# Performance work log

Hardware: AMD Instinct MI355X
Metric: run time of the kernel (lower is better)

## Reference

```python
import jax, jax.numpy as jnp
import numpy as np

N_NODES = 2000
N_EDGES = 32000
B, T = 16, 20
OUT = 8      # GAT out_feats (num_heads=1)
HID = 24     # LSTM hidden
FC_OUT = 160  # num_airports * prediction_horizon = 20*8
FCC_OUT = 20
NEG_SLOPE = 0.2


def setup_inputs() -> dict:
    key = jax.random.key(0)
    ks = jax.random.split(key, 20)
    s = 0.1
    return {
        "x": jax.random.normal(ks[0], (B, T, N_NODES, 1), jnp.float32),
        "edge_w": jax.random.uniform(ks[1], (B, T, N_EDGES, 1), jnp.float32),
        "src": jax.random.randint(ks[2], (N_EDGES,), 0, N_NODES, dtype=jnp.int32),
        "dst": jax.random.randint(ks[3], (N_EDGES,), 0, N_NODES, dtype=jnp.int32),
        # EdgeGATConv params
        "W_node": jax.random.normal(ks[4], (1, OUT), jnp.float32) * s,
        "W_edge": jax.random.normal(ks[5], (1, OUT), jnp.float32) * s,
        "attn_l": jax.random.normal(ks[6], (OUT,), jnp.float32) * s,
        "attn_e": jax.random.normal(ks[7], (OUT,), jnp.float32) * s,
        "attn_r": jax.random.normal(ks[8], (OUT,), jnp.float32) * s,
        "gat_b": jnp.zeros((OUT,), jnp.float32),
        # LSTM params (PyTorch gate order i,f,g,o)
        "w_ih": jax.random.normal(ks[9], (4 * HID, OUT), jnp.float32) * s,
        "w_hh": jax.random.normal(ks[10], (4 * HID, HID), jnp.float32) * s,
        "b_ih": jnp.zeros((4 * HID,), jnp.float32),
        "b_hh": jnp.zeros((4 * HID,), jnp.float32),
        # fc / fcc
        "fc_w": jax.random.normal(ks[11], (FC_OUT, HID), jnp.float32) * s,
        "fc_b": jnp.zeros((FC_OUT,), jnp.float32),
        "fcc_w": jax.random.normal(ks[12], (FCC_OUT, 8 * 20), jnp.float32) * s,
        "fcc_b": jnp.zeros((FCC_OUT,), jnp.float32),
    }


def _gat_graph(xg, wg, src, dst, W_node, W_edge, attn_l, attn_e, attn_r, gat_b):
    # xg: [N,1], wg: [E,1] -> pooled graph feature [OUT]
    fs = xg @ W_node                      # [N,OUT] projected node feats
    fe = wg @ W_edge                      # [E,OUT] projected edge feats
    el = fs @ attn_l                      # [N]
    er = fs @ attn_r                      # [N]  (dst == src features, homogeneous graph)
    ee = fe @ attn_e                      # [E]
    e = jax.nn.leaky_relu(el[src] + ee + er[dst], NEG_SLOPE)  # [E]
    # edge_softmax over incoming edges of each dst node
    emax = jax.ops.segment_max(e, dst, num_segments=N_NODES)  # [N]
    num = jnp.exp(e - emax[dst])
    den = jax.ops.segment_sum(num, dst, num_segments=N_NODES)
    a = num / den[dst]                    # [E]
    msg = a[:, None] * (fs[src] + fe)     # [E,OUT]
    rst = jax.ops.segment_sum(msg, dst, num_segments=N_NODES) + gat_b  # [N,OUT]
    return rst.mean(axis=0)               # graph mean-pool -> [OUT]


def reference(x, edge_w, src, dst, W_node, W_edge, attn_l, attn_e, attn_r, gat_b,
              w_ih, w_hh, b_ih, b_hh, fc_w, fc_b, fcc_w, fcc_b):
    # GAT per (series, time) graph, vmapped over flattened B*T axis
    xf = x.reshape(B * T, N_NODES, 1)
    wf = edge_w.reshape(B * T, N_EDGES, 1)
    gat = jax.vmap(lambda xg, wg: _gat_graph(xg, wg, src, dst, W_node, W_edge,
                                             attn_l, attn_e, attn_r, gat_b))
    feats = gat(xf, wf).reshape(B, T, OUT)  # [B,T,8]
    # Dropout(0.1) -> identity in eval mode

    # LSTM (batch_first), zero initial state
    def step(carry, xt):
        h, c = carry
        g = xt @ w_ih.T + h @ w_hh.T + b_ih + b_hh  # [B,4H]
        i, f, gg, o = jnp.split(g, 4, axis=-1)
        c = jax.nn.sigmoid(f) * c + jax.nn.sigmoid(i) * jnp.tanh(gg)
        h = jax.nn.sigmoid(o) * jnp.tanh(c)
        return (h, c), h

    h0 = jnp.zeros((B, HID), feats.dtype)
    (_, _), hs = jax.lax.scan(step, (h0, h0), jnp.swapaxes(feats, 0, 1))
    outputs = jnp.swapaxes(hs, 0, 1)      # [B,T,24]; squeeze(0) is a no-op for B>1

    out = outputs @ fc_w.T + fc_b         # [B,T,160]
    out = out.reshape(-1, 8 * 20) @ fcc_w.T + fcc_b  # [B*T,20]
    return out
```

## Files before the change

kernel.cpp:

```cpp
#include <hip/hip_runtime.h>
#include <math.h>

#define N_NODES 2000
#define N_EDGES 32000
#define BB 16
#define TT 20
#define NG (BB*TT)
#define OUTF 8
#define HID 24
#define FC_OUTD 160
#define FCC_OUTD 20

#define SC_DEN 4194304.0f
#define SC_T1  1048576.0f
#define SC_T2  4194304.0f



__global__ __launch_bounds__(1024) void gat_fused(
    const float* __restrict__ x, const float* __restrict__ edge_w,
    const int* __restrict__ src, const int* __restrict__ dst,
    const float* __restrict__ W_node, const float* __restrict__ W_edge,
    const float* __restrict__ attn_l, const float* __restrict__ attn_e,
    const float* __restrict__ attn_r, const float* __restrict__ gat_b,
    const float* __restrict__ fc_w, const float* __restrict__ fc_b,
    const float* __restrict__ fcc_w, const float* __restrict__ fcc_b,
    float* __restrict__ ws)
{
    __shared__ float xs[N_NODES];
    __shared__ int   aden[N_NODES];
    __shared__ int   at1[N_NODES];
    __shared__ int   at2[N_NODES];
    __shared__ double wr1[16], wr2[16];

    const int tid = threadIdx.x;

    if (blockIdx.x == NG) {
        if (tid < FCC_OUTD * HID) {
            int j = tid / HID, h = tid % HID;
            float acc = 0.f;
#pragma unroll 4
            for (int m = 0; m < FC_OUTD; ++m)
                acc += fcc_w[j * FC_OUTD + m] * fc_w[m * HID + h];
            ws[NG * OUTF + tid] = acc;
        } else if (tid < FCC_OUTD * HID + FCC_OUTD) {
            int j = tid - FCC_OUTD * HID;
            float acc = fcc_b[j];
#pragma unroll 4
            for (int m = 0; m < FC_OUTD; ++m)
                acc += fcc_w[j * FC_OUTD + m] * fc_b[m];
            ws[NG * OUTF + FCC_OUTD * HID + j] = acc;
        }
        return;
    }

    const int g = blockIdx.x;

    float cl = 0.f, ce = 0.f, cr = 0.f;
#pragma unroll
    for (int k = 0; k < OUTF; ++k) {
        cl += W_node[k] * attn_l[k];
        cr += W_node[k] * attn_r[k];
        ce += W_edge[k] * attn_e[k];
    }

    const float* xg = x + (size_t)g * N_NODES;
    const float* wg = edge_w + (size_t)g * N_EDGES;

    {
        const float4* xg4 = (const float4*)xg;
        for (int i = tid; i < N_NODES/4; i += 1024)
            ((float4*)xs)[i] = xg4[i];
        for (int i = tid; i < N_NODES; i += 1024) {
            aden[i] = 0; at1[i] = 0; at2[i] = 0;
        }
    }
    __syncthreads();

    const int4*   src4 = (const int4*)src;
    const int4*   dst4 = (const int4*)dst;
    const float4* wg4  = (const float4*)wg;
#pragma unroll
    for (int k = 0; k < (N_EDGES/4 + 1023) / 1024; ++k) {
        int c = tid + k * 1024;
        if (c < N_EDGES/4) {
            int4   sv = src4[c];
            int4   dv = dst4[c];
            float4 wv = wg4[c];
#pragma unroll
            for (int j = 0; j < 4; ++j) {
                int   s = (&sv.x)[j];
                int   d = (&dv.x)[j];
                float w = (&wv.x)[j];
                float xsv = xs[s];
                float ev  = cl * xsv + ce * w + cr * xs[d];
                ev = fmaxf(ev, 0.2f * ev);
                float num = __expf(ev);
                atomicAdd(&aden[d], __float2int_rn(num * SC_DEN));
                atomicAdd(&at1[d],  __float2int_rn(num * xsv * SC_T1));
                atomicAdd(&at2[d],  __float2int_rn(num * w * SC_T2));
            }
        }
    }
    __syncthreads();

    double s1 = 0.0, s2 = 0.0;
    for (int n = tid; n < N_NODES; n += 1024) {
        int deni = aden[n];
        if (deni > 0) {
            double inv = 1.0 / (double)deni;
            s1 += (double)at1[n] * 4.0 * inv;
            s2 += (double)at2[n] * inv;
        }
    }
#pragma unroll
    for (int off = 32; off > 0; off >>= 1) {
        s1 += __shfl_down(s1, off, 64);
        s2 += __shfl_down(s2, off, 64);
    }
    int wave = tid >> 6, lane = tid & 63;
    if (lane == 0) { wr1[wave] = s1; wr2[wave] = s2; }
    __syncthreads();
    if (tid == 0) {
        double a = 0.0, c = 0.0;
#pragma unroll
        for (int w = 0; w < 16; ++w) { a += wr1[w]; c += wr2[w]; }
#pragma unroll
        for (int k = 0; k < OUTF; ++k)
            ws[g * OUTF + k] = gat_b[k] +
                (float)((a * (double)W_node[k] + c * (double)W_edge[k]) / (double)N_NODES);
    }
}


__device__ __forceinline__ float fast_sigmoid(float v) {
    return 1.f / (1.f + __expf(-v));
}
__device__ __forceinline__ float fast_tanh(float v) {
    float t = __expf(2.f * v);
    return (t - 1.f) / (t + 1.f);
}

__global__ __launch_bounds__(128) void lstm_head(
    const float* __restrict__ ws,
    const float* __restrict__ w_ih, const float* __restrict__ w_hh,
    const float* __restrict__ b_ih, const float* __restrict__ b_hh,
    float* __restrict__ out)
{
    __shared__ float s_M[FCC_OUTD * HID];
    __shared__ float s_b2[FCC_OUTD];
    __shared__ float s_xt[TT * OUTF];
    __shared__ float s_bias[96];
    __shared__ float s_xg[TT * 96];
    __shared__ float s_g[96];
    __shared__ float s_h[HID], s_c[HID];
    __shared__ float s_hs[TT * HID];

    const int b   = blockIdx.x;
    const int tid = threadIdx.x;

    for (int i = tid; i < FCC_OUTD * HID; i += 128) s_M[i]  = ws[NG * OUTF + i];
    if (tid < FCC_OUTD) s_b2[tid] = ws[NG * OUTF + FCC_OUTD * HID + tid];
    for (int i = tid; i < TT * OUTF; i += 128) s_xt[i] = ws[b * TT * OUTF + i];
    if (tid < 96) s_bias[tid] = b_ih[tid] + b_hh[tid];
    if (tid < HID) { s_h[tid] = 0.f; s_c[tid] = 0.f; }

    float rw_hh[HID];
    if (tid < 96) {
#pragma unroll
        for (int k = 0; k < HID; ++k) rw_hh[k] = w_hh[tid * HID + k];
    }
    __syncthreads();

    for (int u = tid; u < TT * 96; u += 128) {
        int t = u / 96, j = u % 96;
        float acc = s_bias[j];
        const float* xt = &s_xt[t * OUTF];
#pragma unroll
        for (int k = 0; k < OUTF; ++k) acc += xt[k] * w_ih[j * OUTF + k];
        s_xg[u] = acc;
    }
    __syncthreads();

    for (int t = 0; t < TT; ++t) {
        if (tid < 96) {
            float acc = s_xg[t * 96 + tid];
#pragma unroll
            for (int k = 0; k < HID; ++k) acc += s_h[k] * rw_hh[k];
            s_g[tid] = acc;
        }
        __syncthreads();
        if (tid < HID) {
            float i_ = fast_sigmoid(s_g[tid]);
            float f_ = fast_sigmoid(s_g[24 + tid]);
            float g_ = fast_tanh(s_g[48 + tid]);
            float o_ = fast_sigmoid(s_g[72 + tid]);
            float c = f_ * s_c[tid] + i_ * g_;
            s_c[tid] = c;
            float h = o_ * fast_tanh(c);
            s_h[tid] = h;
            s_hs[t * HID + tid] = h;
        }
        __syncthreads();
    }

    for (int u = tid; u < TT * FCC_OUTD; u += 128) {
        int t = u / FCC_OUTD, j = u % FCC_OUTD;
        float acc = s_b2[j];
        const float* hr = &s_hs[t * HID];
#pragma unroll
        for (int h = 0; h < HID; ++h) acc += hr[h] * s_M[j * HID + h];
        out[(b * TT + t) * FCC_OUTD + j] = acc;
    }
}

extern "C" void kernel_launch(void* const* d_in, const int* in_sizes, int n_in,
                              void* d_out, int out_size, void* d_ws, size_t ws_size,
                              hipStream_t stream) {
    const float* x      = (const float*)d_in[0];
    const float* edge_w = (const float*)d_in[1];
    const int*   src    = (const int*)d_in[2];
    const int*   dst    = (const int*)d_in[3];
    const float* W_node = (const float*)d_in[4];
    const float* W_edge = (const float*)d_in[5];
    const float* attn_l = (const float*)d_in[6];
    const float* attn_e = (const float*)d_in[7];
    const float* attn_r = (const float*)d_in[8];
    const float* gat_b  = (const float*)d_in[9];
    const float* w_ih   = (const float*)d_in[10];
    const float* w_hh   = (const float*)d_in[11];
    const float* b_ih   = (const float*)d_in[12];
    const float* b_hh   = (const float*)d_in[13];
    const float* fc_w   = (const float*)d_in[14];
    const float* fc_b   = (const float*)d_in[15];
    const float* fcc_w  = (const float*)d_in[16];
    const float* fcc_b  = (const float*)d_in[17];

    float* ws  = (float*)d_ws;
    float* out = (float*)d_out;

    gat_fused<<<NG + 1, 1024, 0, stream>>>(x, edge_w, src, dst, W_node, W_edge,
                                           attn_l, attn_e, attn_r, gat_b,
                                           fc_w, fc_b, fcc_w, fcc_b, ws);
    lstm_head<<<BB, 128, 0, stream>>>(ws, w_ih, w_hh, b_ih, b_hh, out);
}
```

Baseline: 45.82 us.

## Replace LDS atomic scatter with per-call CSR build and segmented reduction

Adds two small kernels that build a dst-sorted CSR layout each call: a histogram plus prefix scan, then a scatter that records each edge's sorted position and packed src/dst/head-flag metadata. The GAT kernel scatters edge weights into LDS in sorted order and has 1000 threads each reduce 32 consecutive edges with float accumulators. Partial segments that cross thread boundaries are stitched afterwards, replacing the three fixed-point LDS atomics per edge. This trades atomic contention for two extra launches, a 128KB LDS buffer per block that limits occupancy, and only 1000 of 1024 threads active in the main loop.

```diff
diff --git a/kernel.cpp b/kernel.cpp
--- a/kernel.cpp
+++ b/kernel.cpp
@@ -10,51 +10,99 @@
 #define HID 24
 #define FC_OUTD 160
 #define FCC_OUTD 20
-
-#define SC_DEN 4194304.0f
-#define SC_T1  1048576.0f
-#define SC_T2  4194304.0f
-
-
-
-__global__ __launch_bounds__(1024) void gat_fused(
-    const float* __restrict__ x, const float* __restrict__ edge_w,
+#define EPT 32
+#define NTE (N_EDGES/EPT)
+
+#define WS_CSRPOS   0
+#define WS_META     131072
+#define WS_ROWPTR   262144
+#define WS_CURSOR   270336
+#define WS_FEATS    278528
+#define WS_M        290816
+#define WS_B2       292864
+
+
+__global__ __launch_bounds__(1024) void build_hist_scan(
+    const int* __restrict__ dst, int* __restrict__ row_ptr, int* __restrict__ cursor)
+{
+    __shared__ int a[2048], b[2048];
+    const int tid = threadIdx.x;
+    a[tid] = 0; a[tid + 1024] = 0;
+    __syncthreads();
+    for (int e = tid; e < N_EDGES; e += 1024) atomicAdd(&a[dst[e]], 1);
+    __syncthreads();
+    int *s = a, *d = b;
+    for (int off = 1; off < 2048; off <<= 1) {
+        d[tid] = s[tid] + (tid >= off ? s[tid - off] : 0);
+        const int j = tid + 1024;
+        d[j] = s[j] + (j >= off ? s[j - off] : 0);
+        __syncthreads();
+        int* t = s; s = d; d = t;
+    }
+    if (tid == 0) row_ptr[0] = 0;
+    for (int i = tid; i < N_NODES; i += 1024) {
+        row_ptr[i + 1] = s[i];
+        cursor[i] = 0;
+    }
+}
+
+
+__global__ __launch_bounds__(1024) void build_scatter(
     const int* __restrict__ src, const int* __restrict__ dst,
-    const float* __restrict__ W_node, const float* __restrict__ W_edge,
-    const float* __restrict__ attn_l, const float* __restrict__ attn_e,
-    const float* __restrict__ attn_r, const float* __restrict__ gat_b,
+    const int* __restrict__ row_ptr, int* __restrict__ cursor,
+    unsigned* __restrict__ meta, unsigned* __restrict__ csr_pos,
     const float* __restrict__ fc_w, const float* __restrict__ fc_b,
     const float* __restrict__ fcc_w, const float* __restrict__ fcc_b,
-    float* __restrict__ ws)
+    float* __restrict__ Mout, float* __restrict__ b2out)
 {
-    __shared__ float xs[N_NODES];
-    __shared__ int   aden[N_NODES];
-    __shared__ int   at1[N_NODES];
-    __shared__ int   at2[N_NODES];
-    __shared__ double wr1[16], wr2[16];
-
     const int tid = threadIdx.x;
-
-    if (blockIdx.x == NG) {
+    if (blockIdx.x == 32) {
         if (tid < FCC_OUTD * HID) {
-            int j = tid / HID, h = tid % HID;
+            const int j = tid / HID, h = tid % HID;
             float acc = 0.f;
 #pragma unroll 4
             for (int m = 0; m < FC_OUTD; ++m)
                 acc += fcc_w[j * FC_OUTD + m] * fc_w[m * HID + h];
-            ws[NG * OUTF + tid] = acc;
+            Mout[tid] = acc;
         } else if (tid < FCC_OUTD * HID + FCC_OUTD) {
-            int j = tid - FCC_OUTD * HID;
+            const int j = tid - FCC_OUTD * HID;
             float acc = fcc_b[j];
 #pragma unroll 4
             for (int m = 0; m < FC_OUTD; ++m)
                 acc += fcc_w[j * FC_OUTD + m] * fc_b[m];
-            ws[NG * OUTF + FCC_OUTD * HID + j] = acc;
+            b2out[j] = acc;
         }
         return;
     }
-
-    const int g = blockIdx.x;
+    const int e = blockIdx.x * 1024 + tid;
+    if (e >= N_EDGES) return;
+    const int s = src[e], d = dst[e];
+    const int rp  = row_ptr[d];
+    const int pos = rp + atomicAdd(&cursor[d], 1);
+    const unsigned fl = (pos == rp) ? 1u : 0u;
+    const unsigned m  = (unsigned)s | ((unsigned)d << 11) | (fl << 22);
+    const int t = pos >> 5, i = pos & 31;
+    meta[(((i >> 2) * NTE) + t) * 4 + (i & 3)] = m;
+    csr_pos[e] = (unsigned)pos;
+}
+
+
+__global__ __launch_bounds__(1024) void gat_csr(
+    const float* __restrict__ x, const float* __restrict__ edge_w,
+    const unsigned* __restrict__ csr_pos, const int4* __restrict__ meta4,
+    const float* __restrict__ W_node, const float* __restrict__ W_edge,
+    const float* __restrict__ attn_l, const float* __restrict__ attn_e,
+    const float* __restrict__ attn_r, const float* __restrict__ gat_b,
+    float* __restrict__ feats)
+{
+    __shared__ float wsp[N_EDGES];
+    __shared__ float xs[N_NODES];
+    __shared__ int   hn[NTE];
+    __shared__ float hp0[NTE], hp1[NTE], hp2[NTE];
+    __shared__ double wr1[16], wr2[16];
+
+    const int g   = blockIdx.x;
+    const int tid = threadIdx.x;
 
     float cl = 0.f, ce = 0.f, cr = 0.f;
 #pragma unroll
@@ -64,61 +112,83 @@
         ce += W_edge[k] * attn_e[k];
     }
 
-    const float* xg = x + (size_t)g * N_NODES;
-    const float* wg = edge_w + (size_t)g * N_EDGES;
-
     {
-        const float4* xg4 = (const float4*)xg;
-        for (int i = tid; i < N_NODES/4; i += 1024)
-            ((float4*)xs)[i] = xg4[i];
-        for (int i = tid; i < N_NODES; i += 1024) {
-            aden[i] = 0; at1[i] = 0; at2[i] = 0;
-        }
-    }
-    __syncthreads();
-
-    const int4*   src4 = (const int4*)src;
-    const int4*   dst4 = (const int4*)dst;
-    const float4* wg4  = (const float4*)wg;
-#pragma unroll
-    for (int k = 0; k < (N_EDGES/4 + 1023) / 1024; ++k) {
-        int c = tid + k * 1024;
-        if (c < N_EDGES/4) {
-            int4   sv = src4[c];
-            int4   dv = dst4[c];
-            float4 wv = wg4[c];
-#pragma unroll
-            for (int j = 0; j < 4; ++j) {
-                int   s = (&sv.x)[j];
-                int   d = (&dv.x)[j];
-                float w = (&wv.x)[j];
-                float xsv = xs[s];
-                float ev  = cl * xsv + ce * w + cr * xs[d];
-                ev = fmaxf(ev, 0.2f * ev);
-                float num = __expf(ev);
-                atomicAdd(&aden[d], __float2int_rn(num * SC_DEN));
-                atomicAdd(&at1[d],  __float2int_rn(num * xsv * SC_T1));
-                atomicAdd(&at2[d],  __float2int_rn(num * w * SC_T2));
+        const float4* ew4 = (const float4*)(edge_w + (size_t)g * N_EDGES);
+        const int4*   cp4 = (const int4*)csr_pos;
+#pragma unroll
+        for (int k = 0; k < 8; ++k) {
+            const int c = tid + k * 1024;
+            if (c < N_EDGES / 4) {
+                const float4 wv = ew4[c];
+                const int4   pv = cp4[c];
+                wsp[pv.x] = wv.x; wsp[pv.y] = wv.y; wsp[pv.z] = wv.z; wsp[pv.w] = wv.w;
             }
         }
+        if (tid < N_NODES / 4)
+            ((float4*)xs)[tid] = ((const float4*)(x + (size_t)g * N_NODES))[tid];
     }
     __syncthreads();
 
     double s1 = 0.0, s2 = 0.0;
-    for (int n = tid; n < N_NODES; n += 1024) {
-        int deni = aden[n];
-        if (deni > 0) {
-            double inv = 1.0 / (double)deni;
-            s1 += (double)at1[n] * 4.0 * inv;
-            s2 += (double)at2[n] * inv;
-        }
-    }
+    float den = 0.f, t1 = 0.f, t2 = 0.f;
+    int   cur = -1;
+    int   headdone = 0;
+
+    if (tid < NTE) {
+        const int p0 = tid * EPT;
+        float4 wv; int4 mv;
+#pragma unroll
+        for (int i = 0; i < EPT; ++i) {
+            if ((i & 3) == 0) {
+                wv = *(const float4*)&wsp[p0 + i];
+                mv = meta4[(i >> 2) * NTE + tid];
+            }
+            const float w = ((i & 3) == 0) ? wv.x : ((i & 3) == 1) ? wv.y
+                          : ((i & 3) == 2) ? wv.z : wv.w;
+            const int   m = ((i & 3) == 0) ? mv.x : ((i & 3) == 1) ? mv.y
+                          : ((i & 3) == 2) ? mv.z : mv.w;
+            const int s = m & 2047;
+            const int d = (m >> 11) & 2047;
+            if (m & (1 << 22)) {
+                if (headdone) {
+                    s1 += (double)(t1 / den);
+                    s2 += (double)(t2 / den);
+                } else {
+                    hn[tid] = cur; hp0[tid] = den; hp1[tid] = t1; hp2[tid] = t2;
+                    headdone = 1;
+                }
+                den = 0.f; t1 = 0.f; t2 = 0.f;
+                cur = d;
+            } else if (i == 0) {
+                cur = d;
+            }
+            const float xsv = xs[s];
+            const float ev0 = cl * xsv + ce * w + cr * xs[d];
+            const float ev  = fmaxf(ev0, 0.2f * ev0);
+            const float num = __expf(ev);
+            den += num; t1 += num * xsv; t2 += num * w;
+        }
+        if (!headdone) {
+            hn[tid] = cur; hp0[tid] = den; hp1[tid] = t1; hp2[tid] = t2;
+        }
+    }
+    __syncthreads();
+
+    if (tid < NTE && headdone) {
+        int tn = tid + 1;
+        while (tn < NTE && hn[tn] == cur) {
+            den += hp0[tn]; t1 += hp1[tn]; t2 += hp2[tn]; ++tn;
+        }
+        s1 += (double)(t1 / den);
+        s2 += (double)(t2 / den);
+    }
+
 #pragma unroll
     for (int off = 32; off > 0; off >>= 1) {
         s1 += __shfl_down(s1, off, 64);
         s2 += __shfl_down(s2, off, 64);
     }
-    int wave = tid >> 6, lane = tid & 63;
+    const int wave = tid >> 6, lane = tid & 63;
     if (lane == 0) { wr1[wave] = s1; wr2[wave] = s2; }
     __syncthreads();
     if (tid == 0) {
@@ -127,7 +197,7 @@
         for (int w = 0; w < 16; ++w) { a += wr1[w]; c += wr2[w]; }
 #pragma unroll
         for (int k = 0; k < OUTF; ++k)
-            ws[g * OUTF + k] = gat_b[k] +
+            feats[g * OUTF + k] = gat_b[k] +
                 (float)((a * (double)W_node[k] + c * (double)W_edge[k]) / (double)N_NODES);
     }
 }
@@ -142,7 +212,8 @@
 }
 
 __global__ __launch_bounds__(128) void lstm_head(
-    const float* __restrict__ ws,
+    const float* __restrict__ feats, const float* __restrict__ Mw,
+    const float* __restrict__ b2w,
     const float* __restrict__ w_ih, const float* __restrict__ w_hh,
     const float* __restrict__ b_ih, const float* __restrict__ b_hh,
     float* __restrict__ out)
@@ -159,9 +230,9 @@
     const int b   = blockIdx.x;
     const int tid = threadIdx.x;
 
-    for (int i = tid; i < FCC_OUTD * HID; i += 128) s_M[i]  = ws[NG * OUTF + i];
-    if (tid < FCC_OUTD) s_b2[tid] = ws[NG * OUTF + FCC_OUTD * HID + tid];
-    for (int i = tid; i < TT * OUTF; i += 128) s_xt[i] = ws[b * TT * OUTF + i];
+    for (int i = tid; i < FCC_OUTD * HID; i += 128) s_M[i] = Mw[i];
+    if (tid < FCC_OUTD) s_b2[tid] = b2w[tid];
+    for (int i = tid; i < TT * OUTF; i += 128) s_xt[i] = feats[b * TT * OUTF + i];
     if (tid < 96) s_bias[tid] = b_ih[tid] + b_hh[tid];
     if (tid < HID) { s_h[tid] = 0.f; s_c[tid] = 0.f; }
 
@@ -173,7 +244,7 @@
     __syncthreads();
 
     for (int u = tid; u < TT * 96; u += 128) {
-        int t = u / 96, j = u % 96;
+        const int t = u / 96, j = u % 96;
         float acc = s_bias[j];
         const float* xt = &s_xt[t * OUTF];
 #pragma unroll
@@ -191,13 +262,13 @@
         }
         __syncthreads();
         if (tid < HID) {
-            float i_ = fast_sigmoid(s_g[tid]);
-            float f_ = fast_sigmoid(s_g[24 + tid]);
-            float g_ = fast_tanh(s_g[48 + tid]);
-            float o_ = fast_sigmoid(s_g[72 + tid]);
-            float c = f_ * s_c[tid] + i_ * g_;
+            const float i_ = fast_sigmoid(s_g[tid]);
+            const float f_ = fast_sigmoid(s_g[24 + tid]);
+            const float g_ = fast_tanh(s_g[48 + tid]);
+            const float o_ = fast_sigmoid(s_g[72 + tid]);
+            const float c = f_ * s_c[tid] + i_ * g_;
             s_c[tid] = c;
-            float h = o_ * fast_tanh(c);
+            const float h = o_ * fast_tanh(c);
             s_h[tid] = h;
             s_hs[t * HID + tid] = h;
         }
@@ -205,7 +276,7 @@
     }
 
     for (int u = tid; u < TT * FCC_OUTD; u += 128) {
-        int t = u / FCC_OUTD, j = u % FCC_OUTD;
+        const int t = u / FCC_OUTD, j = u % FCC_OUTD;
         float acc = s_b2[j];
         const float* hr = &s_hs[t * HID];
 #pragma unroll
@@ -236,11 +307,20 @@
     const float* fcc_w  = (const float*)d_in[16];
     const float* fcc_b  = (const float*)d_in[17];
 
-    float* ws  = (float*)d_ws;
-    float* out = (float*)d_out;
-
-    gat_fused<<<NG + 1, 1024, 0, stream>>>(x, edge_w, src, dst, W_node, W_edge,
-                                           attn_l, attn_e, attn_r, gat_b,
-                                           fc_w, fc_b, fcc_w, fcc_b, ws);
-    lstm_head<<<BB, 128, 0, stream>>>(ws, w_ih, w_hh, b_ih, b_hh, out);
-}
+    char* ws = (char*)d_ws;
+    unsigned* csr_pos = (unsigned*)(ws + WS_CSRPOS);
+    unsigned* meta    = (unsigned*)(ws + WS_META);
+    int*      row_ptr = (int*)(ws + WS_ROWPTR);
+    int*      cursor  = (int*)(ws + WS_CURSOR);
+    float*    feats   = (float*)(ws + WS_FEATS);
+    float*    Mw      = (float*)(ws + WS_M);
+    float*    b2w     = (float*)(ws + WS_B2);
+    float*    out     = (float*)d_out;
+
+    build_hist_scan<<<1, 1024, 0, stream>>>(dst, row_ptr, cursor);
+    build_scatter<<<33, 1024, 0, stream>>>(src, dst, row_ptr, cursor, meta, csr_pos,
+                                           fc_w, fc_b, fcc_w, fcc_b, Mw, b2w);
+    gat_csr<<<NG, 1024, 0, stream>>>(x, edge_w, csr_pos, (const int4*)meta,
+                                     W_node, W_edge, attn_l, attn_e, attn_r, gat_b, feats);
+    lstm_head<<<BB, 128, 0, stream>>>(feats, Mw, b2w, w_ih, w_hh, b_ih, b_hh, out);
+}
```

Result: slower. 82.98 us (+81.1%).
